# Kernel tuning notes

Measured on AMD Instinct MI355X. Metric: run time of the kernel, lower is better.

The kernel has to match this reference:

```python
import jax, jax.numpy as jnp
import numpy as np


def segment_softmax(scores, seg, num_segments):
    # numerically stable softmax over edges grouped by destination node
    m = jax.ops.segment_max(scores, seg, num_segments=num_segments)
    e = jnp.exp(scores - m[seg])
    d = jax.ops.segment_sum(e, seg, num_segments=num_segments)
    return e / d[seg]


def setup_inputs() -> dict:
    key = jax.random.key(0)
    ks = jax.random.split(key, 13)
    N, E, D = 50000, 400000, 128
    s = 0.02
    return {
        "x": jax.random.normal(ks[0], (N, D), dtype=jnp.float32),
        "t": jax.random.normal(ks[1], (N, D), dtype=jnp.float32),
        "edge_index": jax.random.randint(ks[2], (2, E), 0, N),
        "W_x": jax.random.normal(ks[3], (D, D), dtype=jnp.float32) * s,
        "W_t": jax.random.normal(ks[4], (D, D), dtype=jnp.float32) * s,
        "Q_alpha_w": jax.random.normal(ks[5], (D, D), dtype=jnp.float32) * s,
        "Q_alpha_b": jax.random.normal(ks[6], (D,), dtype=jnp.float32) * s,
        "K_alpha_w": jax.random.normal(ks[7], (D, D), dtype=jnp.float32) * s,
        "K_alpha_b": jax.random.normal(ks[8], (D,), dtype=jnp.float32) * s,
        "Q_beta_w": jax.random.normal(ks[9], (D, D), dtype=jnp.float32) * s,
        "Q_beta_b": jax.random.normal(ks[10], (D,), dtype=jnp.float32) * s,
        "K_beta_w": jax.random.normal(ks[11], (D, D), dtype=jnp.float32) * s,
        "K_beta_b": jax.random.normal(ks[12], (D,), dtype=jnp.float32) * s,
    }


def reference(x, t, edge_index, W_x, W_t, Q_alpha_w, Q_alpha_b,
              K_alpha_w, K_alpha_b, Q_beta_w, Q_beta_b, K_beta_w, K_beta_b):
    N, D = x.shape
    row, col = edge_index[0], edge_index[1]  # row = dest (i), col = src (j)
    inv_sqrt_d = 1.0 / (D ** 0.5)

    # Linear projections on nodes, then gather per edge (same math as
    # projecting the gathered edge features, since Linear is per-row).
    q_alpha = (t @ Q_alpha_w.T + Q_alpha_b)[row]   # [E, D]
    k_alpha = (t @ K_alpha_w.T + K_alpha_b)[col]   # [E, D]
    alpha_scores = jnp.sum(q_alpha * k_alpha, axis=-1) * inv_sqrt_d  # [E]
    alpha = segment_softmax(alpha_scores, row, N)  # [E]

    q_beta = (x @ Q_beta_w.T + Q_beta_b)[row]
    k_beta = (x @ K_beta_w.T + K_beta_b)[col]
    beta_scores = jnp.sum(q_beta * k_beta, axis=-1) * inv_sqrt_d
    beta = segment_softmax(beta_scores, row, N)

    msg_for_t = alpha[:, None] * (t @ W_t.T)[col]  # [E, D]
    msg_for_x = beta[:, None] * (x @ W_x.T)[col]   # [E, D]

    out_x = jax.ops.segment_sum(msg_for_x, row, num_segments=N)  # [N, D]
    out_t = jax.ops.segment_sum(msg_for_t, row, num_segments=N)  # [N, D]
    return (out_x, out_t)
```

## Files before the change

### kernel.cpp

```cpp
#include <hip/hip_runtime.h>

__device__ __forceinline__ unsigned short f2bf(float f) {
    unsigned int x = __float_as_uint(f);
    x += 0x7fffu + ((x >> 16) & 1u);
    return (unsigned short)(x >> 16);
}
__device__ __forceinline__ float2 bf2x(unsigned int u) {
    float2 r;
    r.x = __uint_as_float(u << 16);
    r.y = __uint_as_float(u & 0xffff0000u);
    return r;
}
template <int PAT>
__device__ __forceinline__ float swzadd(float v) {
    return v + __uint_as_float(__builtin_amdgcn_ds_swizzle(__float_as_uint(v), PAT));
}

typedef __attribute__((ext_vector_type(8))) short frag8;
typedef __attribute__((ext_vector_type(4))) float fragf4;


__global__ __launch_bounds__(256) void prep_convert_hist(
    const float* __restrict__ Qa_w, const float* __restrict__ Ka_w,
    const float* __restrict__ Qa_b,
    const float* __restrict__ Qb_w, const float* __restrict__ Kb_w,
    const float* __restrict__ Qb_b,
    const float* __restrict__ W_t, const float* __restrict__ W_x,
    unsigned short* __restrict__ Wbf, float* __restrict__ ba, float* __restrict__ bb,
    const int* __restrict__ row, int* __restrict__ deg, int E)
{
    const int b = blockIdx.x;
    const int tid = threadIdx.x;
    const float sc = 0.08838834764831845f;

    if (b < 32) {
        const int m = b >> 4;
        const int ro = b & 15;
        const float* Kw = m ? Kb_w : Ka_w;
        const float* Qw = m ? Qb_w : Qa_w;
        const int r = ro * 8 + (tid >> 5);
        const int c0 = (tid & 31) * 4;
        float a0 = 0.f, a1 = 0.f, a2 = 0.f, a3 = 0.f;
#pragma unroll 4
        for (int ch = 0; ch < 128; ch++) {
            const float kv = Kw[ch * 128 + r];
            const float4 q = *(const float4*)(Qw + ch * 128 + c0);
            a0 = fmaf(kv, q.x, a0); a1 = fmaf(kv, q.y, a1);
            a2 = fmaf(kv, q.z, a2); a3 = fmaf(kv, q.w, a3);
        }
        const int ct = r >> 4, li = r & 15;
        const int ks = c0 >> 5, quad = (c0 >> 3) & 3, j = c0 & 7;
        ushort4 u;
        u.x = f2bf(a0 * sc); u.y = f2bf(a1 * sc);
        u.z = f2bf(a2 * sc); u.w = f2bf(a3 * sc);
        *(ushort4*)(Wbf + (size_t)m * 16384 +
                    ((size_t)((ct * 4 + ks) * 64 + quad * 16 + li)) * 8 + j) = u;
    } else if (b < 34) {
        const int m = b - 32;
        if (tid < 128) {
            const float* Kw = m ? Kb_w : Ka_w;
            const float* bq = m ? Qb_b : Qa_b;
            float a = 0.f;
#pragma unroll 4
            for (int ch = 0; ch < 128; ch++) a = fmaf(bq[ch], Kw[ch * 128 + tid], a);
            (m ? bb : ba)[tid] = a * sc;
        }
    } else if (b < 66) {
        const int cm = (b - 34) >> 4;
        const int local = (b - 34) & 15;
        const int id = local * 256 + tid;
        const int e4 = id * 4;
        const float* s = cm ? W_x : W_t;
        float4 v = *(const float4*)(s + e4);
        int r = e4 >> 7, c = e4 & 127;
        int ct = r >> 4, li = r & 15;
        int ks = c >> 5, quad = (c >> 3) & 3, j = c & 7;
        ushort4 u;
        u.x = f2bf(v.x); u.y = f2bf(v.y); u.z = f2bf(v.z); u.w = f2bf(v.w);
        *(ushort4*)(Wbf + (size_t)(2 + cm) * 16384 +
                    ((size_t)((ct * 4 + ks) * 64 + quad * 16 + li)) * 8 + j) = u;
    } else {
        int e = (b - 66) * 256 + tid;
        if (e < E) atomicAdd(&deg[row[e]], 1);
    }
}

#define TLROW 72
__global__ __launch_bounds__(256, 4) void proj_scatter(
    const float* __restrict__ in_t, const float* __restrict__ in_x, int N,
    const unsigned short* __restrict__ Wbf,
    const float* __restrict__ ba, const float* __restrict__ bb,
    unsigned short* __restrict__ q2ab, unsigned short* __restrict__ txb,
    const int* __restrict__ erow, const int* __restrict__ ecol,
    int* __restrict__ cursor, int* __restrict__ csr_col, int E,
    int nScat, int nbx)
{
    __shared__ __align__(16) unsigned short tile[4][16 * TLROW];

    if ((int)blockIdx.x < nScat) {
        int e = blockIdx.x * 256 + threadIdx.x;
        if (e < E) {
            int p = atomicAdd(&cursor[erow[e]], 1);
            csr_col[p] = ecol[e];
        }
        return;
    }
    const int pb = blockIdx.x - nScat;
    const int bx = pb % nbx;
    const int rest = pb / nbx;
    const int p = rest & 1;
    const int cth = rest >> 1;

    const int wave = threadIdx.x >> 6;
    const int lane = threadIdx.x & 63;
    const int li = lane & 15, quad = lane >> 4;
    const int r0 = (bx * 4 + wave) * 16;
    if (r0 >= N) return;
    const int r = r0 + li;
    const bool rv = r < N;

    frag8 bt[4];
    {
        const float* inp = p ? in_x : in_t;
        const float* st = inp + (size_t)r * 128 + quad * 8;
#pragma unroll
        for (int ks = 0; ks < 4; ks++) {
            float4 lo = make_float4(0.f, 0.f, 0.f, 0.f), hi = lo;
            if (rv) {
                lo = *(const float4*)(st + ks * 32);
                hi = *(const float4*)(st + ks * 32 + 4);
            }
            frag8 f;
            f[0] = (short)f2bf(lo.x); f[1] = (short)f2bf(lo.y);
            f[2] = (short)f2bf(lo.z); f[3] = (short)f2bf(lo.w);
            f[4] = (short)f2bf(hi.x); f[5] = (short)f2bf(hi.y);
            f[6] = (short)f2bf(hi.z); f[7] = (short)f2bf(hi.w);
            bt[ks] = f;
        }
    }

    if (cth == 0 && rv) {
#pragma unroll
        for (int ks = 0; ks < 4; ks++)
            *(frag8*)(txb + (size_t)r * 256 + p * 128 + ks * 32 + quad * 8) = bt[ks];
    }

    const unsigned short* wb = Wbf + (size_t)p * 16384 + (size_t)cth * 8192
                             + (size_t)lane * 8;
    frag8 af[16];
#pragma unroll
    for (int u = 0; u < 16; u++)
        af[u] = *(const frag8*)(wb + u * 512);

    fragf4 acc[4];
#pragma unroll
    for (int ct = 0; ct < 4; ct++) acc[ct] = (fragf4){0.f, 0.f, 0.f, 0.f};
#pragma unroll
    for (int ct = 0; ct < 4; ct++) {
#pragma unroll
        for (int ks = 0; ks < 4; ks++)
            acc[ct] = __builtin_amdgcn_mfma_f32_16x16x32_bf16(
                af[ct * 4 + ks], bt[ks], acc[ct], 0, 0, 0);
    }

    const float* bias = (p ? bb : ba) + cth * 64;
    unsigned short* lt = &tile[wave][0];
#pragma unroll
    for (int ct = 0; ct < 4; ct++) {
        const int c = ct * 16 + quad * 4;
        float4 bv = *(const float4*)(bias + c);
        ushort4 u;
        u.x = f2bf(acc[ct][0] + bv.x);
        u.y = f2bf(acc[ct][1] + bv.y);
        u.z = f2bf(acc[ct][2] + bv.z);
        u.w = f2bf(acc[ct][3] + bv.w);
        *(ushort4*)&lt[li * TLROW + c] = u;
    }
    const int coff = p * 128 + cth * 64;
#pragma unroll
    for (int it = 0; it < 2; it++) {
        const int rr = it * 8 + (lane >> 3);
        const int cg = lane & 7;
        if (r0 + rr < N) {
            uint4 v = *(const uint4*)&lt[rr * TLROW + cg * 8];
            *(uint4*)(q2ab + (size_t)(r0 + rr) * 256 + coff + cg * 8) = v;
        }
    }
}

#define SCAN_CHUNK 2048

__device__ __forceinline__ int wave_incl_scan(int v, int lane) {
#pragma unroll
    for (int d = 1; d < 64; d <<= 1) {
        int u = __shfl_up(v, d, 64);
        if (lane >= d) v += u;
    }
    return v;
}

__global__ __launch_bounds__(256) void scan_partial(const int* __restrict__ deg,
                                                    int* __restrict__ partial, int N) {
    const int tid = threadIdx.x;
    const int base = blockIdx.x * SCAN_CHUNK + tid * 8;
    int s = 0;
#pragma unroll
    for (int j = 0; j < 8; j++) {
        int i = base + j;
        s += (i < N) ? deg[i] : 0;
    }
    const int lane = tid & 63;
    s = wave_incl_scan(s, lane);
    __shared__ int wsum[4];
    if (lane == 63) wsum[tid >> 6] = s;
    __syncthreads();
    if (tid == 0) partial[blockIdx.x] = wsum[0] + wsum[1] + wsum[2] + wsum[3];
}

__global__ __launch_bounds__(64) void scan_base(int* __restrict__ partial, int nb,
                                                int* __restrict__ offs, int N) {
    const int lane = threadIdx.x;
    int v = (lane < nb) ? partial[lane] : 0;
    int inc = wave_incl_scan(v, lane);
    if (lane < nb) partial[lane] = inc - v;
    if (lane == 63) offs[N] = inc;
}

__global__ __launch_bounds__(256) void scan_final(const int* __restrict__ deg,
                                                  const int* __restrict__ partial,
                                                  int* __restrict__ offs,
                                                  int* __restrict__ cursor, int N) {
    const int tid = threadIdx.x;
    const int lane = tid & 63;
    const int wv = tid >> 6;
    const int base = blockIdx.x * SCAN_CHUNK + tid * 8;
    int v[8];
    int s = 0;
#pragma unroll
    for (int j = 0; j < 8; j++) {
        int i = base + j;
        v[j] = (i < N) ? deg[i] : 0;
        s += v[j];
    }
    int incl = wave_incl_scan(s, lane);
    __shared__ int wsum[4];
    if (lane == 63) wsum[wv] = incl;
    __syncthreads();
    int wbase = 0;
#pragma unroll
    for (int w = 0; w < 4; w++) wbase += (w < wv) ? wsum[w] : 0;
    int run = partial[blockIdx.x] + wbase + incl - s;
#pragma unroll
    for (int j = 0; j < 8; j++) {
        int i = base + j;
        if (i < N) { offs[i] = run; cursor[i] = run; }
        run += v[j];
    }
}

__global__ __launch_bounds__(256) void edge_fused(
    const unsigned short* __restrict__ q2ab, const unsigned short* __restrict__ txb,
    const unsigned short* __restrict__ Wbf,
    const int* __restrict__ csr_col, const int* __restrict__ offs,
    float* __restrict__ out_x, float* __restrict__ out_t, int N)
{
    __shared__ __align__(16) unsigned short tile[16][264];
    const int tid = threadIdx.x;
    const int wv = tid >> 6, lane = tid & 63;
    const int g = lane >> 4, sub = lane & 15;
    const int nblk = blockIdx.x * 16;
    if (nblk >= N) return;
    const int n = nblk + wv * 4 + g;
    const bool nv = n < N;

    float qa_r[8], qb_r[8];
    if (nv) {
        uint4 a = *(const uint4*)(q2ab + (size_t)n * 256 + sub * 8);
        uint4 b = *(const uint4*)(q2ab + (size_t)n * 256 + 128 + sub * 8);
        float2 f;
        f = bf2x(a.x); qa_r[0] = f.x; qa_r[1] = f.y;
        f = bf2x(a.y); qa_r[2] = f.x; qa_r[3] = f.y;
        f = bf2x(a.z); qa_r[4] = f.x; qa_r[5] = f.y;
        f = bf2x(a.w); qa_r[6] = f.x; qa_r[7] = f.y;
        f = bf2x(b.x); qb_r[0] = f.x; qb_r[1] = f.y;
        f = bf2x(b.y); qb_r[2] = f.x; qb_r[3] = f.y;
        f = bf2x(b.z); qb_r[4] = f.x; qb_r[5] = f.y;
        f = bf2x(b.w); qb_r[6] = f.x; qb_r[7] = f.y;
    } else {
#pragma unroll
        for (int j = 0; j < 8; j++) { qa_r[j] = 0.f; qb_r[j] = 0.f; }
    }

    int s = 0, e = 0;
    if (nv) { s = offs[n]; e = offs[n + 1]; }

    float aggt[8], aggx[8];
#pragma unroll
    for (int j = 0; j < 8; j++) { aggt[j] = 0.f; aggx[j] = 0.f; }
    float dda = 0.f, ddb = 0.f;

    if (e > s) {
        int c = csr_col[s];
        const unsigned short* rp = txb + (size_t)c * 256;
        uint4 t8 = *(const uint4*)(rp + sub * 8);
        uint4 x8 = *(const uint4*)(rp + 128 + sub * 8);
        for (int i = s; i < e; i++) {
            const int inx = (i + 1 < e) ? i + 1 : i;
            const int cn = csr_col[inx];
            const unsigned short* rn = txb + (size_t)cn * 256;
            uint4 t8n = *(const uint4*)(rn + sub * 8);
            uint4 x8n = *(const uint4*)(rn + 128 + sub * 8);

            float tv[8], xv[8];
            float2 f;
            f = bf2x(t8.x); tv[0] = f.x; tv[1] = f.y;
            f = bf2x(t8.y); tv[2] = f.x; tv[3] = f.y;
            f = bf2x(t8.z); tv[4] = f.x; tv[5] = f.y;
            f = bf2x(t8.w); tv[6] = f.x; tv[7] = f.y;
            f = bf2x(x8.x); xv[0] = f.x; xv[1] = f.y;
            f = bf2x(x8.y); xv[2] = f.x; xv[3] = f.y;
            f = bf2x(x8.z); xv[4] = f.x; xv[5] = f.y;
            f = bf2x(x8.w); xv[6] = f.x; xv[7] = f.y;

            float pa = 0.f, pb = 0.f;
#pragma unroll
            for (int j = 0; j < 8; j++) {
                pa = fmaf(qa_r[j], tv[j], pa);
                pb = fmaf(qb_r[j], xv[j], pb);
            }
            pa = swzadd<0x041F>(pa); pb = swzadd<0x041F>(pb);
            pa = swzadd<0x081F>(pa); pb = swzadd<0x081F>(pb);
            pa = swzadd<0x101F>(pa); pb = swzadd<0x101F>(pb);
            pa = swzadd<0x201F>(pa); pb = swzadd<0x201F>(pb);

            const float ea = __expf(fminf(pa, 60.f));
            const float eb = __expf(fminf(pb, 60.f));
            dda += ea; ddb += eb;
#pragma unroll
            for (int j = 0; j < 8; j++) {
                aggt[j] = fmaf(ea, tv[j], aggt[j]);
                aggx[j] = fmaf(eb, xv[j], aggx[j]);
            }
            t8 = t8n; x8 = x8n;
        }
    }

    const float ra = (dda > 0.f) ? 1.f / dda : 0.f;
    const float rb = (ddb > 0.f) ? 1.f / ddb : 0.f;
    const int rowi = wv * 4 + g;
    frag8 ut, ux;
#pragma unroll
    for (int j = 0; j < 8; j++) {
        ut[j] = (short)f2bf(aggt[j] * ra);
        ux[j] = (short)f2bf(aggx[j] * rb);
    }
    *(frag8*)&tile[rowi][sub * 8] = ut;
    *(frag8*)&tile[rowi][128 + sub * 8] = ux;
    __syncthreads();

    const int m = wv >> 1, chunk = wv & 1;
    const int li = lane & 15, quad = lane >> 4;
    frag8 bt[4];
#pragma unroll
    for (int ks = 0; ks < 4; ks++)
        bt[ks] = *(const frag8*)&tile[li][m * 128 + ks * 32 + quad * 8];
    const unsigned short* wbp = Wbf + (size_t)(2 + m) * 16384 + (size_t)chunk * 8192
                              + (size_t)lane * 8;
    frag8 af[16];
#pragma unroll
    for (int u = 0; u < 16; u++)
        af[u] = *(const frag8*)(wbp + u * 512);
    fragf4 acc[4];
#pragma unroll
    for (int ct = 0; ct < 4; ct++) acc[ct] = (fragf4){0.f, 0.f, 0.f, 0.f};
#pragma unroll
    for (int ct = 0; ct < 4; ct++) {
#pragma unroll
        for (int ks = 0; ks < 4; ks++)
            acc[ct] = __builtin_amdgcn_mfma_f32_16x16x32_bf16(
                af[ct * 4 + ks], bt[ks], acc[ct], 0, 0, 0);
    }
    if (nblk + li < N) {
        float* outp = (m ? out_x : out_t) + (size_t)(nblk + li) * 128 + chunk * 64;
#pragma unroll
        for (int ct = 0; ct < 4; ct++)
            *(float4*)(outp + ct * 16 + quad * 4) =
                make_float4(acc[ct][0], acc[ct][1], acc[ct][2], acc[ct][3]);
    }
}

extern "C" void kernel_launch(void* const* d_in, const int* in_sizes, int n_in,
                              void* d_out, int out_size, void* d_ws, size_t ws_size,
                              hipStream_t stream) {
    const float* x    = (const float*)d_in[0];
    const float* t    = (const float*)d_in[1];
    const int*   ei   = (const int*)d_in[2];
    const float* W_x  = (const float*)d_in[3];
    const float* W_t  = (const float*)d_in[4];
    const float* Qa_w = (const float*)d_in[5];
    const float* Qa_b = (const float*)d_in[6];
    const float* Ka_w = (const float*)d_in[7];
    const float* Qb_w = (const float*)d_in[9];
    const float* Qb_b = (const float*)d_in[10];
    const float* Kb_w = (const float*)d_in[11];

    const int N = in_sizes[0] / 128;
    const int E = in_sizes[2] / 2;
    const int* row = ei;
    const int* col = ei + E;

    char* ws = (char*)d_ws;
    size_t off = 0;
    auto carve = [&](size_t bytes) -> void* {
        void* p = ws + off;
        off += (bytes + 255) & ~(size_t)255;
        return p;
    };
    unsigned short* q2ab = (unsigned short*)carve((size_t)N * 256 * 2);
    unsigned short* txb  = (unsigned short*)carve((size_t)N * 256 * 2);
    int* deg      = (int*)carve((size_t)N * 4);
    int* cursor   = (int*)carve((size_t)N * 4);
    int* offs     = (int*)carve((size_t)(N + 1) * 4);
    int* csr_col  = (int*)carve((size_t)E * 4);
    const int nscan = (N + SCAN_CHUNK - 1) / SCAN_CHUNK;
    int* partial  = (int*)carve((size_t)nscan * 4);
    unsigned short* Wbf = (unsigned short*)carve((size_t)4 * 16384 * 2);
    float* ba = (float*)carve(128 * 4);
    float* bb = (float*)carve(128 * 4);

    (void)hipMemsetAsync(deg, 0, (size_t)N * 4, stream);

    dim3 b256(256);
    const int nHist = (E + 255) / 256;
    prep_convert_hist<<<dim3(66 + nHist), b256, 0, stream>>>(
        Qa_w, Ka_w, Qa_b, Qb_w, Kb_w, Qb_b, W_t, W_x, Wbf, ba, bb, row, deg, E);

    scan_partial<<<dim3(nscan), b256, 0, stream>>>(deg, partial, N);
    scan_base<<<dim3(1), dim3(64), 0, stream>>>(partial, nscan, offs, N);
    scan_final<<<dim3(nscan), b256, 0, stream>>>(deg, partial, offs, cursor, N);

    const int nbx = (N + 63) / 64;
    const int nScat = (E + 255) / 256;
    proj_scatter<<<dim3(nScat + nbx * 4), b256, 0, stream>>>(
        t, x, N, Wbf, ba, bb, q2ab, txb,
        row, col, cursor, csr_col, E, nScat, nbx);

    float* out_x = (float*)d_out;
    float* out_t = out_x + (size_t)N * 128;
    edge_fused<<<dim3((N + 15) / 16), b256, 0, stream>>>(
        q2ab, txb, Wbf, csr_col, offs, out_x, out_t, N);
}
```

Baseline: 256.6 us.

## Merge three scan kernels into one and deepen edge gather prefetch to two

Replaces the three-kernel exclusive scan over node degrees with a single kernel. Each block recomputes its prefix by reducing all preceding degree entries directly, and offs[N] is set to E. The per-node edge loop in edge_fused now keeps two edges of gathered rows in flight instead of one, to hide gather latency. The costs are redundant prefix reads in later scan blocks and extra registers for the deeper prefetch, which could lower occupancy.

Result: no change. 261.2 us (+1.8%).

```diff
diff --git a/kernel.cpp b/kernel.cpp
--- a/kernel.cpp
+++ b/kernel.cpp
@@ -85,6 +85,64 @@
     }
 }
 
+#define SCAN_CHUNK 2048
+
+__device__ __forceinline__ int wave_incl_scan(int v, int lane) {
+#pragma unroll
+    for (int d = 1; d < 64; d <<= 1) {
+        int u = __shfl_up(v, d, 64);
+        if (lane >= d) v += u;
+    }
+    return v;
+}
+
+__global__ __launch_bounds__(256) void scan_all(
+    const int* __restrict__ deg, int* __restrict__ offs,
+    int* __restrict__ cursor, int N, int E)
+{
+    const int tid = threadIdx.x;
+    const int lane = tid & 63;
+    const int wv = tid >> 6;
+    __shared__ int wred[4];
+    __shared__ int wsum[4];
+
+    const int lim = blockIdx.x * SCAN_CHUNK;
+    int pre = 0;
+    for (int idx = tid * 4; idx < lim; idx += 1024) {
+        const int4 v4 = *(const int4*)(deg + idx);
+        pre += v4.x + v4.y + v4.z + v4.w;
+    }
+#pragma unroll
+    for (int d = 1; d < 64; d <<= 1) pre += __shfl_xor(pre, d, 64);
+    if (lane == 0) wred[wv] = pre;
+
+    if (blockIdx.x == 0 && tid == 0) offs[N] = E;
+
+    const int base0 = blockIdx.x * SCAN_CHUNK + tid * 8;
+    int v[8];
+    int ssum = 0;
+#pragma unroll
+    for (int j = 0; j < 8; j++) {
+        int i = base0 + j;
+        v[j] = (i < N) ? deg[i] : 0;
+        ssum += v[j];
+    }
+    int incl = wave_incl_scan(ssum, lane);
+    if (lane == 63) wsum[wv] = incl;
+    __syncthreads();
+    const int base = wred[0] + wred[1] + wred[2] + wred[3];
+    int wbase = 0;
+#pragma unroll
+    for (int w = 0; w < 4; w++) wbase += (w < wv) ? wsum[w] : 0;
+    int run = base + wbase + incl - ssum;
+#pragma unroll
+    for (int j = 0; j < 8; j++) {
+        int i = base0 + j;
+        if (i < N) { offs[i] = run; cursor[i] = run; }
+        run += v[j];
+    }
+}
+
 #define TLROW 72
 __global__ __launch_bounds__(256, 4) void proj_scatter(
     const float* __restrict__ in_t, const float* __restrict__ in_x, int N,
@@ -185,76 +243,6 @@
             uint4 v = *(const uint4*)&lt[rr * TLROW + cg * 8];
             *(uint4*)(q2ab + (size_t)(r0 + rr) * 256 + coff + cg * 8) = v;
         }
-    }
-}
-
-#define SCAN_CHUNK 2048
-
-__device__ __forceinline__ int wave_incl_scan(int v, int lane) {
-#pragma unroll
-    for (int d = 1; d < 64; d <<= 1) {
-        int u = __shfl_up(v, d, 64);
-        if (lane >= d) v += u;
-    }
-    return v;
-}
-
-__global__ __launch_bounds__(256) void scan_partial(const int* __restrict__ deg,
-                                                    int* __restrict__ partial, int N) {
-    const int tid = threadIdx.x;
-    const int base = blockIdx.x * SCAN_CHUNK + tid * 8;
-    int s = 0;
-#pragma unroll
-    for (int j = 0; j < 8; j++) {
-        int i = base + j;
-        s += (i < N) ? deg[i] : 0;
-    }
-    const int lane = tid & 63;
-    s = wave_incl_scan(s, lane);
-    __shared__ int wsum[4];
-    if (lane == 63) wsum[tid >> 6] = s;
-    __syncthreads();
-    if (tid == 0) partial[blockIdx.x] = wsum[0] + wsum[1] + wsum[2] + wsum[3];
-}
-
-__global__ __launch_bounds__(64) void scan_base(int* __restrict__ partial, int nb,
-                                                int* __restrict__ offs, int N) {
-    const int lane = threadIdx.x;
-    int v = (lane < nb) ? partial[lane] : 0;
-    int inc = wave_incl_scan(v, lane);
-    if (lane < nb) partial[lane] = inc - v;
-    if (lane == 63) offs[N] = inc;
-}
-
-__global__ __launch_bounds__(256) void scan_final(const int* __restrict__ deg,
-                                                  const int* __restrict__ partial,
-                                                  int* __restrict__ offs,
-                                                  int* __restrict__ cursor, int N) {
-    const int tid = threadIdx.x;
-    const int lane = tid & 63;
-    const int wv = tid >> 6;
-    const int base = blockIdx.x * SCAN_CHUNK + tid * 8;
-    int v[8];
-    int s = 0;
-#pragma unroll
-    for (int j = 0; j < 8; j++) {
-        int i = base + j;
-        v[j] = (i < N) ? deg[i] : 0;
-        s += v[j];
-    }
-    int incl = wave_incl_scan(s, lane);
-    __shared__ int wsum[4];
-    if (lane == 63) wsum[wv] = incl;
-    __syncthreads();
-    int wbase = 0;
-#pragma unroll
-    for (int w = 0; w < 4; w++) wbase += (w < wv) ? wsum[w] : 0;
-    int run = partial[blockIdx.x] + wbase + incl - s;
-#pragma unroll
-    for (int j = 0; j < 8; j++) {
-        int i = base + j;
-        if (i < N) { offs[i] = run; cursor[i] = run; }
-        run += v[j];
     }
 }
 
@@ -300,27 +288,32 @@
     float dda = 0.f, ddb = 0.f;
 
     if (e > s) {
-        int c = csr_col[s];
-        const unsigned short* rp = txb + (size_t)c * 256;
-        uint4 t8 = *(const uint4*)(rp + sub * 8);
-        uint4 x8 = *(const uint4*)(rp + 128 + sub * 8);
+        const int e1 = e - 1;
+        const int c0i = csr_col[s];
+        const int c1i = csr_col[(s + 1 < e) ? s + 1 : e1];
+        const unsigned short* rp0 = txb + (size_t)c0i * 256;
+        const unsigned short* rp1 = txb + (size_t)c1i * 256;
+        uint4 t0 = *(const uint4*)(rp0 + sub * 8);
+        uint4 x0 = *(const uint4*)(rp0 + 128 + sub * 8);
+        uint4 t1 = *(const uint4*)(rp1 + sub * 8);
+        uint4 x1 = *(const uint4*)(rp1 + 128 + sub * 8);
         for (int i = s; i < e; i++) {
-            const int inx = (i + 1 < e) ? i + 1 : i;
-            const int cn = csr_col[inx];
-            const unsigned short* rn = txb + (size_t)cn * 256;
-            uint4 t8n = *(const uint4*)(rn + sub * 8);
-            uint4 x8n = *(const uint4*)(rn + 128 + sub * 8);
+            const int i2 = i + 2;
+            const int c2 = csr_col[(i2 < e) ? i2 : e1];
+            const unsigned short* rp2 = txb + (size_t)c2 * 256;
+            const uint4 t2 = *(const uint4*)(rp2 + sub * 8);
+            const uint4 x2 = *(const uint4*)(rp2 + 128 + sub * 8);
 
             float tv[8], xv[8];
             float2 f;
-            f = bf2x(t8.x); tv[0] = f.x; tv[1] = f.y;
-            f = bf2x(t8.y); tv[2] = f.x; tv[3] = f.y;
-            f = bf2x(t8.z); tv[4] = f.x; tv[5] = f.y;
-            f = bf2x(t8.w); tv[6] = f.x; tv[7] = f.y;
-            f = bf2x(x8.x); xv[0] = f.x; xv[1] = f.y;
-            f = bf2x(x8.y); xv[2] = f.x; xv[3] = f.y;
-            f = bf2x(x8.z); xv[4] = f.x; xv[5] = f.y;
-            f = bf2x(x8.w); xv[6] = f.x; xv[7] = f.y;
+            f = bf2x(t0.x); tv[0] = f.x; tv[1] = f.y;
+            f = bf2x(t0.y); tv[2] = f.x; tv[3] = f.y;
+            f = bf2x(t0.z); tv[4] = f.x; tv[5] = f.y;
+            f = bf2x(t0.w); tv[6] = f.x; tv[7] = f.y;
+            f = bf2x(x0.x); xv[0] = f.x; xv[1] = f.y;
+            f = bf2x(x0.y); xv[2] = f.x; xv[3] = f.y;
+            f = bf2x(x0.z); xv[4] = f.x; xv[5] = f.y;
+            f = bf2x(x0.w); xv[6] = f.x; xv[7] = f.y;
 
             float pa = 0.f, pb = 0.f;
 #pragma unroll
@@ -341,7 +334,7 @@
                 aggt[j] = fmaf(ea, tv[j], aggt[j]);
                 aggx[j] = fmaf(eb, xv[j], aggx[j]);
             }
-            t8 = t8n; x8 = x8n;
+            t0 = t1; x0 = x1; t1 = t2; x1 = x2;
         }
     }
 
@@ -422,8 +415,6 @@
     int* cursor   = (int*)carve((size_t)N * 4);
     int* offs     = (int*)carve((size_t)(N + 1) * 4);
     int* csr_col  = (int*)carve((size_t)E * 4);
-    const int nscan = (N + SCAN_CHUNK - 1) / SCAN_CHUNK;
-    int* partial  = (int*)carve((size_t)nscan * 4);
     unsigned short* Wbf = (unsigned short*)carve((size_t)4 * 16384 * 2);
     float* ba = (float*)carve(128 * 4);
     float* bb = (float*)carve(128 * 4);
@@ -435,9 +426,8 @@
     prep_convert_hist<<<dim3(66 + nHist), b256, 0, stream>>>(
         Qa_w, Ka_w, Qa_b, Qb_w, Kb_w, Qb_b, W_t, W_x, Wbf, ba, bb, row, deg, E);
 
-    scan_partial<<<dim3(nscan), b256, 0, stream>>>(deg, partial, N);
-    scan_base<<<dim3(1), dim3(64), 0, stream>>>(partial, nscan, offs, N);
-    scan_final<<<dim3(nscan), b256, 0, stream>>>(deg, partial, offs, cursor, N);
+    const int nscan = (N + SCAN_CHUNK - 1) / SCAN_CHUNK;
+    scan_all<<<dim3(nscan), b256, 0, stream>>>(deg, offs, cursor, N, E);
 
     const int nbx = (N + 63) / 64;
     const int nScat = (E + 255) / 256;
```
